# Kernel tuning notes

Hardware: AMD Instinct MI355X
Metric: run time of the kernel (lower is better)

Reference implementation:

```python
import jax, jax.numpy as jnp
import numpy as np

D_MODEL = 2048
N_HEADS = 16
D_K = D_MODEL // N_HEADS
MAX_SEQ_LEN = 2048


def _rotary_tables(dim, max_seq_len):
    angular_freq = (1.0 / 10000.0) ** jnp.linspace(0.0, 1.0, dim // 2, dtype=jnp.float32)
    t = jnp.arange(max_seq_len, dtype=jnp.float32)
    theta = jnp.einsum('i,j->ij', t, angular_freq)  # [S, dk/2]
    return jnp.cos(theta), jnp.sin(theta)


def _apply_rotary(x, cos, sin):
    # x: [B, H, S, dk]; cos/sin: [S, dk/2]
    seq_len = x.shape[-2]
    c = cos[:seq_len][None, None]
    s = sin[:seq_len][None, None]
    x1, x2 = jnp.split(x, 2, axis=-1)
    y1 = x1 * c - x2 * s
    y2 = x1 * s + x2 * c
    return jnp.concatenate([y1, y2], axis=-1).astype(x.dtype)


def setup_inputs() -> dict:
    key = jax.random.key(0)
    k_x, k_qkv, k_o = jax.random.split(key, 3)
    B, S = 2, 2048
    x = jax.random.normal(k_x, (B, S, D_MODEL), dtype=jnp.float32)
    scale = 1.0 / np.sqrt(D_MODEL)
    w_qkv = jax.random.normal(k_qkv, (3 * D_MODEL, D_MODEL), dtype=jnp.float32) * scale
    w_o = jax.random.normal(k_o, (D_MODEL, D_MODEL), dtype=jnp.float32) * scale
    return {"x": x, "w_qkv": w_qkv, "w_o": w_o}


def reference(x, w_qkv, w_o):
    B, S, _ = x.shape
    cos, sin = _rotary_tables(D_K, MAX_SEQ_LEN)
    qkv = jnp.einsum('bsd,ed->bse', x, w_qkv)  # [B, S, 3*d_model]
    qkv = qkv.reshape(B, S, 3, N_HEADS, D_K).transpose(2, 0, 3, 1, 4)  # [3,B,H,S,dk]
    Q, K, V = qkv[0], qkv[1], qkv[2]
    Q = _apply_rotary(Q, cos, sin)
    K = _apply_rotary(K, cos, sin)
    scale = 1.0 / np.sqrt(D_K)
    scores = jnp.einsum('bhqd,bhkd->bhqk', Q, K) * scale
    causal = jnp.tril(jnp.ones((S, S), dtype=bool))
    scores = jnp.where(causal[None, None], scores, jnp.finfo(scores.dtype).min)
    attn = jax.nn.softmax(scores, axis=-1)
    out = jnp.einsum('bhqk,bhkd->bhqd', attn, V)  # [B,H,S,dk]
    out = out.transpose(0, 2, 1, 3).reshape(B, S, D_MODEL)
    return jnp.einsum('bsd,ed->bse', out, w_o)
```

## Files before the change

kernel.cpp:

```cpp
#include <hip/hip_runtime.h>
#include <hip/hip_bf16.h>


typedef __bf16 bf16;
typedef __bf16 bf16x4 __attribute__((ext_vector_type(4)));
typedef __bf16 bf16x8 __attribute__((ext_vector_type(8)));
typedef float f32x4 __attribute__((ext_vector_type(4)));
typedef float f32x16 __attribute__((ext_vector_type(16)));
typedef int i32x4 __attribute__((ext_vector_type(4)));

#define DEV __device__ __forceinline__

DEV void gll16(const void* g, void* lds_base_wave_uniform) {
  __builtin_amdgcn_global_load_lds((const __attribute__((address_space(1))) void*)g,
                                   (__attribute__((address_space(3))) void*)lds_base_wave_uniform,
                                   16, 0, 0);
}

DEV f32x4 mfma16(bf16x8 a, bf16x8 b, f32x4 c) {
  return __builtin_amdgcn_mfma_f32_16x16x32_bf16(a, b, c, 0, 0, 0);
}
DEV f32x16 mfma32(bf16x8 a, bf16x8 b, f32x16 c) {
  return __builtin_amdgcn_mfma_f32_32x32x16_bf16(a, b, c, 0, 0, 0);
}

DEV int cvtpk(float lo, float hi) {
  int r;
  asm("v_cvt_pk_bf16_f32 %0, %1, %2" : "=v"(r) : "v"(lo), "v"(hi));
  return r;
}

__global__ __launch_bounds__(256) void prep_all(const float* __restrict__ x,
                                                const float* __restrict__ wqkv,
                                                const float* __restrict__ wo,
                                                bf16* __restrict__ xb,
                                                bf16* __restrict__ wqkvb,
                                                bf16* __restrict__ wob,
                                                float* __restrict__ ctab,
                                                float* __restrict__ stab) {
  const int b = blockIdx.x;
  if (b < 12288) {
    const float* in;
    bf16* out;
    int bb = b;
    if (b < 4096) {
      in = x; out = xb;
    } else if (b < 10240) {
      in = wqkv; out = wqkvb; bb -= 4096;
    } else {
      in = wo; out = wob; bb -= 10240;
    }
    const int i = (bb * 256 + threadIdx.x) << 3;
    float4 a = *(const float4*)(in + i);
    float4 c = *(const float4*)(in + i + 4);
    bf16x8 o;
    o[0] = (bf16)a.x; o[1] = (bf16)a.y; o[2] = (bf16)a.z; o[3] = (bf16)a.w;
    o[4] = (bf16)c.x; o[5] = (bf16)c.y; o[6] = (bf16)c.z; o[7] = (bf16)c.w;
    *(bf16x8*)(out + i) = o;
  } else {
    const int id = (b - 12288) * 256 + threadIdx.x;
    const int s = id >> 6, j = id & 63;
    float freq = powf(10000.0f, -(float)j / 63.0f);
    float th = (float)s * freq;
    ctab[id] = cosf(th);
    stab[id] = sinf(th);
  }
}

__global__ __launch_bounds__(512, 2) void gemm384(const bf16* __restrict__ A,
                                                  const bf16* __restrict__ Bt,
                                                  bf16* __restrict__ q_out,
                                                  bf16* __restrict__ k_out,
                                                  bf16* __restrict__ v_out,
                                                  const float* __restrict__ ctab,
                                                  const float* __restrict__ stab) {
  constexpr int K = 2048, NKT = 64;
  constexpr int BUFB = 40960;
  __shared__ char lds[3 * BUFB];
  const int id = blockIdx.x;
  const int swz = (id & 7) * 32 + (id >> 3);
  const int bx = swz & 15, by = swz >> 4;
  const int m0 = by << 8;
  const int n0 = bx * 384;
  const int tid = threadIdx.x, w = tid >> 6, l = tid & 63;
  const int wm = w >> 2, wn = w & 3;
  const int lsl = (l & 7) ^ ((l >> 3) & 7);
  const int srow = ((l >> 3) << 1) + (lsl >> 2);
  const int scol = (lsl & 3) << 3;

  auto STAGE = [&](int t, char* base) {
    const int k0 = t << 5;
#pragma unroll
    for (int c = 0; c < 2; ++c) {
      const int row = (c << 7) + (w << 4) + srow;
      gll16(A + (size_t)(m0 + row) * K + k0 + scol, base + (c << 13) + (w << 10));
    }
#pragma unroll
    for (int c = 0; c < 3; ++c) {
      const int row = (c << 7) + (w << 4) + srow;
      gll16(Bt + (size_t)(n0 + row) * K + k0 + scol, base + 16384 + (c << 13) + (w << 10));
    }
  };

  f32x4 acc[8][6] = {};

  STAGE(0, (char*)lds);
  STAGE(1, (char*)lds + BUFB);
  asm volatile("s_waitcnt vmcnt(5)" ::: "memory");
  __builtin_amdgcn_s_barrier();

#pragma unroll 1
  for (int t = 0, bi = 0, bj = 2; t < NKT; ++t) {
    char* rbase = (char*)lds + bi * BUFB;
    bf16x8 bfr[6];
#pragma unroll
    for (int j = 0; j < 6; ++j) {
      const int row = ((j >> 1) << 7) + ((j & 1) << 6) + (wn << 4) + (l & 15);
      const int sr = row >> 1;
      bfr[j] = *(const bf16x8*)(rbase + 16384 + sr * 128 +
                                (((((row & 1) << 2) | (l >> 4)) ^ (sr & 7)) << 4));
    }
    bf16x8 af[4];
#pragma unroll
    for (int i = 0; i < 4; ++i) {
      const int row = (wm << 7) + (i << 4) + (l & 15);
      const int sr = row >> 1;
      af[i] = *(const bf16x8*)(rbase + sr * 128 +
                               (((((row & 1) << 2) | (l >> 4)) ^ (sr & 7)) << 4));
    }
    if (t + 2 < NKT) STAGE(t + 2, (char*)lds + bj * BUFB);
    asm volatile("s_waitcnt lgkmcnt(0)" ::: "memory");
    __builtin_amdgcn_sched_barrier(0);
    __builtin_amdgcn_s_setprio(1);
#pragma unroll
    for (int i = 0; i < 4; ++i)
#pragma unroll
      for (int j = 0; j < 6; ++j)
        acc[i][j] = mfma16(af[i], bfr[j], acc[i][j]);
    __builtin_amdgcn_s_setprio(0);
#pragma unroll
    for (int i = 0; i < 4; ++i) {
      const int row = (wm << 7) + 64 + (i << 4) + (l & 15);
      const int sr = row >> 1;
      af[i] = *(const bf16x8*)(rbase + sr * 128 +
                               (((((row & 1) << 2) | (l >> 4)) ^ (sr & 7)) << 4));
    }
    asm volatile("s_waitcnt lgkmcnt(0)" ::: "memory");
    __builtin_amdgcn_sched_barrier(0);
    __builtin_amdgcn_s_setprio(1);
#pragma unroll
    for (int i = 0; i < 4; ++i)
#pragma unroll
      for (int j = 0; j < 6; ++j)
        acc[4 + i][j] = mfma16(af[i], bfr[j], acc[4 + i][j]);
    __builtin_amdgcn_s_setprio(0);
    if (t + 2 < NKT) {
      asm volatile("s_waitcnt vmcnt(5)" ::: "memory");
    } else if (t + 2 == NKT) {
      asm volatile("s_waitcnt vmcnt(0)" ::: "memory");
    }
    __builtin_amdgcn_sched_barrier(0);
    __builtin_amdgcn_s_barrier();
    bi = (bi == 2) ? 0 : bi + 1;
    bj = (bj == 2) ? 0 : bj + 1;
  }

  const int d2 = (wn << 4) + (l & 15);
#pragma unroll
  for (int i = 0; i < 8; ++i) {
    const int mbase = m0 + (wm << 7) + (i << 4) + ((l >> 4) << 2);
    const int b_ = mbase >> 11, sbase = mbase & 2047;
    float cc[4], ss[4];
    if (((n0 + 256) >> 11) == 1 || (n0 >> 11) == 1) {
#pragma unroll
      for (int r = 0; r < 4; ++r) {
        cc[r] = ctab[((sbase + r) << 6) + d2];
        ss[r] = stab[((sbase + r) << 6) + d2];
      }
    }
#pragma unroll
    for (int p = 0; p < 3; ++p) {
      const int nb = n0 + (p << 7);
      const int which = nb >> 11;
      const int h = (nb >> 7) & 15;
      if (which == 0) {
        const size_t base = (((size_t)((b_ << 4) | h)) * 2048 + sbase) * 128;
#pragma unroll
        for (int r = 0; r < 4; ++r) {
          q_out[base + ((size_t)r << 7) + d2]      = (bf16)acc[i][2 * p][r];
          q_out[base + ((size_t)r << 7) + d2 + 64] = (bf16)acc[i][2 * p + 1][r];
        }
      } else if (which == 1) {
        const size_t base = (((size_t)((b_ << 4) | h)) * 2048 + sbase) * 128;
#pragma unroll
        for (int r = 0; r < 4; ++r) {
          const float x1 = acc[i][2 * p][r], x2 = acc[i][2 * p + 1][r];
          k_out[base + ((size_t)r << 7) + d2]      = (bf16)(x1 * cc[r] - x2 * ss[r]);
          k_out[base + ((size_t)r << 7) + d2 + 64] = (bf16)(x1 * ss[r] + x2 * cc[r]);
        }
      } else {
        bf16x4 v1, v2;
#pragma unroll
        for (int r = 0; r < 4; ++r) {
          v1[r] = (bf16)acc[i][2 * p][r];
          v2[r] = (bf16)acc[i][2 * p + 1][r];
        }
        const size_t hb = ((size_t)((b_ << 4) | h) << 18);
        *(bf16x4*)(v_out + hb + ((size_t)d2 << 11) + sbase) = v1;
        *(bf16x4*)(v_out + hb + ((size_t)(d2 + 64) << 11) + sbase) = v2;
      }
    }
  }
}

template <int NTN>
__global__ __launch_bounds__(256, 2) void gemm_o(const bf16* __restrict__ A,
                                                 const bf16* __restrict__ Bt,
                                                 float* __restrict__ f_out) {
  constexpr int K = 2048, NKT = 64;
  constexpr int BUFB = 16384;
  __shared__ char lds[3 * BUFB];
  const int nwg = 32 * NTN;
  const int id = blockIdx.x;
  const int swz = (id & 7) * (nwg >> 3) + (id >> 3);
  const int bx = swz % NTN, by = swz / NTN;
  const int m0 = by << 7, n0 = bx << 7;
  const int tid = threadIdx.x, w = tid >> 6, l = tid & 63;
  const int wm = w >> 1, wn = w & 1;
  const int lsl = (l & 7) ^ ((l >> 3) & 7);
  const int srow = ((l >> 3) << 1) + (lsl >> 2);
  const int scol = (lsl & 3) << 3;

  auto STAGE = [&](int t, char* base) {
    const int k0 = t << 5;
#pragma unroll
    for (int c = 0; c < 2; ++c) {
      const int row = (c << 6) + (w << 4) + srow;
      gll16(A + (size_t)(m0 + row) * K + k0 + scol, base + (c << 12) + (w << 10));
      gll16(Bt + (size_t)(n0 + row) * K + k0 + scol, base + 8192 + (c << 12) + (w << 10));
    }
  };

  f32x4 acc[4][4] = {};

  STAGE(0, (char*)lds);
  STAGE(1, (char*)lds + BUFB);
  asm volatile("s_waitcnt vmcnt(4)" ::: "memory");
  __builtin_amdgcn_s_barrier();

#pragma unroll 1
  for (int t = 0, bi = 0, bj = 2; t < NKT; ++t) {
    char* rbase = (char*)lds + bi * BUFB;
    bf16x8 af[4], bfr[4];
#pragma unroll
    for (int i = 0; i < 4; ++i) {
      const int row = (wm << 6) + (i << 4) + (l & 15);
      const int sr = row >> 1;
      af[i] = *(const bf16x8*)(rbase + sr * 128 +
                               (((((row & 1) << 2) | (l >> 4)) ^ (sr & 7)) << 4));
    }
#pragma unroll
    for (int j = 0; j < 4; ++j) {
      const int row = (wn << 6) + (j << 4) + (l & 15);
      const int sr = row >> 1;
      bfr[j] = *(const bf16x8*)(rbase + 8192 + sr * 128 +
                                (((((row & 1) << 2) | (l >> 4)) ^ (sr & 7)) << 4));
    }
    if (t + 2 < NKT) STAGE(t + 2, (char*)lds + bj * BUFB);
    asm volatile("s_waitcnt lgkmcnt(0)" ::: "memory");
    __builtin_amdgcn_sched_barrier(0);
    __builtin_amdgcn_s_setprio(1);
#pragma unroll
    for (int i = 0; i < 4; ++i)
#pragma unroll
      for (int j = 0; j < 4; ++j)
        acc[i][j] = mfma16(af[i], bfr[j], acc[i][j]);
    __builtin_amdgcn_s_setprio(0);
    if (t + 2 < NKT) {
      asm volatile("s_waitcnt vmcnt(4)" ::: "memory");
    } else if (t + 2 == NKT) {
      asm volatile("s_waitcnt vmcnt(0)" ::: "memory");
    }
    __builtin_amdgcn_sched_barrier(0);
    __builtin_amdgcn_s_barrier();
    bi = (bi == 2) ? 0 : bi + 1;
    bj = (bj == 2) ? 0 : bj + 1;
  }

#pragma unroll
  for (int i = 0; i < 4; ++i)
#pragma unroll
    for (int j = 0; j < 4; ++j)
#pragma unroll
      for (int r = 0; r < 4; ++r) {
        const int m = m0 + (wm << 6) + (i << 4) + ((l >> 4) << 2) + r;
        const int n = n0 + (wn << 6) + (j << 4) + (l & 15);
        f_out[(size_t)m * 2048 + n] = acc[i][j][r];
      }
}

__global__ __launch_bounds__(512, 2) void attn_kernel(const bf16* __restrict__ Qb,
                                                      const bf16* __restrict__ Kb,
                                                      const bf16* __restrict__ Vt,
                                                      bf16* __restrict__ Ao,
                                                      const float* __restrict__ ctab,
                                                      const float* __restrict__ stab) {
  constexpr int S = 2048;
  __shared__ char lds[2][65536];
  const int id = blockIdx.x;
  const int swz = (id & 7) * 32 + (id >> 3);
  const int bh = swz >> 3;
  const int pp = swz & 7;
  const int ntA = pp + 1;
  const int NT = 17;
  const int tid = threadIdx.x, w = tid >> 6, l = tid & 63;
  const int wq = w & 3, half = w >> 2;
  const int hi = l >> 5;
  const bf16* Qp = Qb + ((size_t)bh << 18);
  const bf16* Kp = Kb + ((size_t)bh << 18);
  const bf16* Vp = Vt + ((size_t)bh << 18);

  auto KVSEQ = [&](int ti) { return ((ti < ntA) ? ti : ti - ntA) << 7; };

  auto STAGE_KV = [&](int kv0, int bufi) {
    char* Kbase = lds[bufi];
    char* Vbase = lds[bufi] + 32768;
#pragma unroll
    for (int i = 0; i < 2; ++i) {
      const int rk = (w << 4) + (i << 3) + ((l >> 4) << 1) + (i == 0 ? 0 : 0);
      (void)rk;
    }
#pragma unroll
    for (int i = 0; i < 2; ++i) {
    }
#pragma unroll
    for (int i = 0; i < 2; ++i) {
      const int r0 = (w << 4) + (i << 3) + (l >> 4);
      const int r1 = r0 + 4;
      gll16(Kp + ((size_t)(kv0 + r0) << 7) + (((l & 15) ^ (r0 & 7)) << 3),
            Kbase + (w << 12) + (i << 11));
      gll16(Kp + ((size_t)(kv0 + r1) << 7) + (((l & 15) ^ (r1 & 7)) << 3),
            Kbase + (w << 12) + (i << 11) + 1024);
      gll16(Vp + (size_t)r0 * S + kv0 + (((l & 15) ^ (r0 & 7)) << 3),
            Vbase + (w << 12) + (i << 11));
      gll16(Vp + (size_t)r1 * S + kv0 + (((l & 15) ^ (r1 & 7)) << 3),
            Vbase + (w << 12) + (i << 11) + 1024);
    }
  };

  bf16x8 qf[8];
  auto LOAD_Q = [&](int q0_) {
    const int sq = q0_ + (wq << 5) + (l & 31);
#pragma unroll
    for (int kt = 0; kt < 8; ++kt)
      qf[kt] = *(const bf16x8*)(Qp + ((size_t)sq << 7) + (kt << 4) + (hi << 3));
    const float QS = 0.08838834764831845f * 1.4426950408889634f;
#pragma unroll
    for (int kt = 0; kt < 4; ++kt) {
      const int d2 = (kt << 4) + (hi << 3);
      const float* cp = ctab + (sq << 6) + d2;
      const float* sp = stab + (sq << 6) + d2;
      float4 c0 = *(const float4*)cp, c1 = *(const float4*)(cp + 4);
      float4 s0 = *(const float4*)sp, s1 = *(const float4*)(sp + 4);
      const float cA[8] = {c0.x, c0.y, c0.z, c0.w, c1.x, c1.y, c1.z, c1.w};
      const float sA[8] = {s0.x, s0.y, s0.z, s0.w, s1.x, s1.y, s1.z, s1.w};
      const bf16x8 lo = qf[kt], up = qf[kt + 4];
#pragma unroll
      for (int j2 = 0; j2 < 8; ++j2) {
        const float a = (float)lo[j2], b2 = (float)up[j2];
        qf[kt][j2]     = (bf16)((a * cA[j2] - b2 * sA[j2]) * QS);
        qf[kt + 4][j2] = (bf16)((a * sA[j2] + b2 * cA[j2]) * QS);
      }
    }
  };

  f32x16 o[4] = {};
  float mrun = -3e38f, lrun = 0.f;
  int q0 = pp << 7;

  auto MERGE_EPI = [&](int q0_, char* scratch) {
    bf16* ob = (bf16*)scratch;
    float* ml = (float*)(scratch + 36864);
    __syncthreads();
    if (half == 1) {
      bf16* dst = ob + ((wq << 6) + l) * 72;
#pragma unroll
      for (int dt = 0; dt < 4; ++dt) {
        bf16x8 t0, t1;
#pragma unroll
        for (int e = 0; e < 8; ++e) { t0[e] = (bf16)o[dt][e]; t1[e] = (bf16)o[dt][8 + e]; }
        *(bf16x8*)(dst + (dt << 4)) = t0;
        *(bf16x8*)(dst + (dt << 4) + 8) = t1;
      }
      if (l < 32) {
        ml[(wq << 5) + l] = mrun;
        ml[128 + (wq << 5) + l] = lrun;
      }
    }
    __syncthreads();
    if (half == 0) {
      const float mhi = ml[(wq << 5) + (l & 31)];
      const float lhi = ml[128 + (wq << 5) + (l & 31)];
      const float ms = fmaxf(mrun, mhi);
      const float alo = exp2f(mrun - ms), ahi = exp2f(mhi - ms);
      const float rinv = 1.0f / (lrun * alo + lhi * ahi);
      const bf16* src = ob + ((wq << 6) + l) * 72;
      const int b = bh >> 4, h = bh & 15;
      const int sq = q0_ + (wq << 5) + (l & 31);
      bf16* Arow = Ao + (((size_t)(b * S + sq)) << 11) + (h << 7);
#pragma unroll
      for (int dt = 0; dt < 4; ++dt) {
        bf16x8 h0 = *(const bf16x8*)(src + (dt << 4));
        bf16x8 h1 = *(const bf16x8*)(src + (dt << 4) + 8);
#pragma unroll
        for (int g = 0; g < 4; ++g) {
          bf16x4 ov;
#pragma unroll
          for (int r = 0; r < 4; ++r) {
            const int e = (g << 2) + r;
            const float hv = (e < 8) ? (float)h0[e] : (float)h1[e - 8];
            ov[r] = (bf16)((o[dt][e] * alo + hv * ahi) * rinv);
          }
          *(bf16x4*)(Arow + (dt << 5) + (g << 3) + (hi << 2)) = ov;
        }
      }
    }
  };

  STAGE_KV(KVSEQ(0), 0);
  LOAD_Q(q0);
  __syncthreads();

  int bufi = 0;
#pragma unroll 1
  for (int ti = 0; ti < NT; ++ti, bufi ^= 1) {
    if (ti + 1 < NT) STAGE_KV(KVSEQ(ti + 1), bufi ^ 1);
    const int kv0 = KVSEQ(ti);
    const int kvh0 = kv0 + (half << 6);
    const int qminw = q0 + (wq << 5);
    if (kvh0 <= qminw + 31) {
      const char* Kbase = lds[bufi];
      const char* Vbase = lds[bufi] + 32768;
      f32x16 sc0 = {}, sc1 = {};
      __builtin_amdgcn_s_setprio(1);
#pragma unroll
      for (int kt = 0; kt < 8; ++kt) {
        const int rk0 = (l & 31) + (half << 6);
        const int coff = (kt << 5) + (hi << 4);
        bf16x8 k0 = *(const bf16x8*)(Kbase + (rk0 << 8) + (coff ^ ((rk0 & 7) << 4)));
        bf16x8 k1 = *(const bf16x8*)(Kbase + ((rk0 + 32) << 8) + (coff ^ (((rk0 + 32) & 7) << 4)));
        sc0 = mfma32(k0, qf[kt], sc0);
        sc1 = mfma32(k1, qf[kt], sc1);
      }
      __builtin_amdgcn_s_setprio(0);
      if (kvh0 + 63 > qminw) {
        const int qg = qminw + (l & 31);
#pragma unroll
        for (int r = 0; r < 16; ++r) {
          const int kvr = kvh0 + (r & 3) + ((r >> 2) << 3) + (hi << 2);
          if (kvr > qg) sc0[r] = -3e38f;
          if (kvr + 32 > qg) sc1[r] = -3e38f;
        }
      }
      f32x16 mm;
#pragma unroll
      for (int r = 0; r < 16; ++r) mm[r] = fmaxf(sc0[r], sc1[r]);
#pragma unroll
      for (int off = 8; off; off >>= 1)
#pragma unroll
        for (int r = 0; r < off; ++r) mm[r] = fmaxf(mm[r], mm[r + off]);
      float mx = mm[0];
      mx = fmaxf(mx, __shfl_xor(mx, 32));
      const float mnew = fmaxf(mrun, mx);
      if (!__all(mx <= mrun)) {
        const float alpha = exp2f(mrun - mnew);
        lrun *= alpha;
#pragma unroll
        for (int dt = 0; dt < 4; ++dt) o[dt] *= alpha;
      }
      mrun = mnew;
      float p0 = 0.f, p1 = 0.f, p2 = 0.f, p3 = 0.f;
#pragma unroll
      for (int r = 0; r < 16; r += 2) {
        sc0[r] = exp2f(sc0[r] - mnew); sc0[r + 1] = exp2f(sc0[r + 1] - mnew);
        sc1[r] = exp2f(sc1[r] - mnew); sc1[r + 1] = exp2f(sc1[r + 1] - mnew);
        p0 += sc0[r]; p1 += sc0[r + 1]; p2 += sc1[r]; p3 += sc1[r + 1];
      }
      float ps = (p0 + p1) + (p2 + p3);
      ps += __shfl_xor(ps, 32);
      lrun += ps;
#pragma unroll
      for (int ks = 0; ks < 4; ++ks) {
        const f32x16& s = (ks & 2) ? sc1 : sc0;
        const int rbp = (ks & 1) << 3;
        int pa_ = cvtpk(s[rbp + 0], s[rbp + 1]);
        int pb_ = cvtpk(s[rbp + 2], s[rbp + 3]);
        int pc_ = cvtpk(s[rbp + 4], s[rbp + 5]);
        int pd_ = cvtpk(s[rbp + 6], s[rbp + 7]);
        int sa = __shfl_xor(pa_, 32), sb2 = __shfl_xor(pb_, 32);
        int sc_ = __shfl_xor(pc_, 32), sd = __shfl_xor(pd_, 32);
        i32x4 pi;
        pi[0] = hi ? sc_ : pa_;
        pi[1] = hi ? sd : pb_;
        pi[2] = hi ? pc_ : sa;
        pi[3] = hi ? pd_ : sb2;
        const bf16x8 pf = __builtin_bit_cast(bf16x8, pi);
        __builtin_amdgcn_s_setprio(1);
#pragma unroll
        for (int dt = 0; dt < 4; ++dt) {
          const int rd = (dt << 5) + (l & 31);
          const int coffv = (half << 7) + (ks << 5) + (hi << 4);
          const bf16x8 vf = *(const bf16x8*)(Vbase + (rd << 8) +
                                             (coffv ^ ((rd & 7) << 4)));
          o[dt] = mfma32(vf, pf, o[dt]);
        }
        __builtin_amdgcn_s_setprio(0);
      }
    }
    if (ti == ntA - 1) {
      MERGE_EPI(q0, lds[bufi]);
      q0 = (15 - pp) << 7;
#pragma unroll
      for (int dt = 0; dt < 4; ++dt)
#pragma unroll
        for (int r = 0; r < 16; ++r) o[dt][r] = 0.f;
      mrun = -3e38f; lrun = 0.f;
      LOAD_Q(q0);
    }
    __syncthreads();
  }
  MERGE_EPI(q0, lds[(NT - 1) & 1]);
}

extern "C" void kernel_launch(void* const* d_in, const int* in_sizes, int n_in,
                              void* d_out, int out_size, void* d_ws, size_t ws_size,
                              hipStream_t stream) {
  const float* x = (const float*)d_in[0];
  const float* w_qkv = (const float*)d_in[1];
  const float* w_o = (const float*)d_in[2];
  float* out = (float*)d_out;
  char* ws = (char*)d_ws;

  bf16* xb    = (bf16*)(ws);
  bf16* wqkvb = (bf16*)(ws + (16ull << 20));
  bf16* wob   = (bf16*)(ws + (40ull << 20));
  bf16* Qb    = (bf16*)(ws + (48ull << 20));
  bf16* Kb    = (bf16*)(ws + (64ull << 20));
  bf16* Vt    = (bf16*)(ws + (80ull << 20));
  bf16* Ao    = (bf16*)(ws + (96ull << 20));
  float* ctab = (float*)(ws + (112ull << 20));
  float* stab = (float*)(ws + (113ull << 20));

  prep_all<<<12800, 256, 0, stream>>>(x, w_qkv, w_o, xb, wqkvb, wob, ctab, stab);
  gemm384<<<256, 512, 0, stream>>>(xb, wqkvb, Qb, Kb, Vt, ctab, stab);
  attn_kernel<<<256, 512, 0, stream>>>(Qb, Kb, Vt, Ao, ctab, stab);
  gemm_o<16><<<512, 256, 0, stream>>>(Ao, wob, out);
}
```

Baseline: 227.4 us.

## Halve attention KV tile to 64 rows to fit more blocks per CU

Shrinks each staged K/V tile from 128 to 64 keys, halving LDS per buffer so four 512-thread blocks can share a CU instead of two, and doubles the number of KV iterations. Each half-block now processes 32 keys with a single score accumulator, which cuts register pressure. The merge scratch is re-laid out with an XOR swizzle, and the max/sum values get their own small shared buffer. The cost is more loop iterations, more barriers and more staging overhead per tile, and the higher occupancy target may force register spills.

```diff
diff --git a/kernel.cpp b/kernel.cpp
--- a/kernel.cpp
+++ b/kernel.cpp
@@ -299,20 +299,21 @@
       }
 }
 
-__global__ __launch_bounds__(512, 2) void attn_kernel(const bf16* __restrict__ Qb,
+__global__ __launch_bounds__(512, 4) void attn_kernel(const bf16* __restrict__ Qb,
                                                       const bf16* __restrict__ Kb,
                                                       const bf16* __restrict__ Vt,
                                                       bf16* __restrict__ Ao,
                                                       const float* __restrict__ ctab,
                                                       const float* __restrict__ stab) {
   constexpr int S = 2048;
-  __shared__ char lds[2][65536];
+  __shared__ char lds[2][32768];
+  __shared__ float mlbuf[256];
   const int id = blockIdx.x;
   const int swz = (id & 7) * 32 + (id >> 3);
   const int bh = swz >> 3;
   const int pp = swz & 7;
-  const int ntA = pp + 1;
-  const int NT = 17;
+  const int ntA = (pp + 1) << 1;
+  const int NT = 34;
   const int tid = threadIdx.x, w = tid >> 6, l = tid & 63;
   const int wq = w & 3, half = w >> 2;
   const int hi = l >> 5;
@@ -320,31 +321,19 @@
   const bf16* Kp = Kb + ((size_t)bh << 18);
   const bf16* Vp = Vt + ((size_t)bh << 18);
 
-  auto KVSEQ = [&](int ti) { return ((ti < ntA) ? ti : ti - ntA) << 7; };
+  auto KVSEQ = [&](int ti) { return ((ti < ntA) ? ti : ti - ntA) << 6; };
 
   auto STAGE_KV = [&](int kv0, int bufi) {
     char* Kbase = lds[bufi];
-    char* Vbase = lds[bufi] + 32768;
+    char* Vbase = lds[bufi] + 16384;
 #pragma unroll
     for (int i = 0; i < 2; ++i) {
-      const int rk = (w << 4) + (i << 3) + ((l >> 4) << 1) + (i == 0 ? 0 : 0);
-      (void)rk;
-    }
-#pragma unroll
-    for (int i = 0; i < 2; ++i) {
-    }
-#pragma unroll
-    for (int i = 0; i < 2; ++i) {
-      const int r0 = (w << 4) + (i << 3) + (l >> 4);
-      const int r1 = r0 + 4;
-      gll16(Kp + ((size_t)(kv0 + r0) << 7) + (((l & 15) ^ (r0 & 7)) << 3),
-            Kbase + (w << 12) + (i << 11));
-      gll16(Kp + ((size_t)(kv0 + r1) << 7) + (((l & 15) ^ (r1 & 7)) << 3),
-            Kbase + (w << 12) + (i << 11) + 1024);
-      gll16(Vp + (size_t)r0 * S + kv0 + (((l & 15) ^ (r0 & 7)) << 3),
-            Vbase + (w << 12) + (i << 11));
-      gll16(Vp + (size_t)r1 * S + kv0 + (((l & 15) ^ (r1 & 7)) << 3),
-            Vbase + (w << 12) + (i << 11) + 1024);
+      const int rk = (w << 3) + (i << 2) + (l >> 4);
+      gll16(Kp + ((size_t)(kv0 + rk) << 7) + (((l & 15) ^ (rk & 7)) << 3),
+            Kbase + (w << 11) + (i << 10));
+      const int rv = (w << 4) + (i << 3) + (l >> 3);
+      gll16(Vp + (size_t)rv * S + kv0 + (((l & 7) ^ (rv & 7)) << 3),
+            Vbase + (w << 11) + (i << 10));
     }
   };
 
@@ -379,39 +368,37 @@
   int q0 = pp << 7;
 
   auto MERGE_EPI = [&](int q0_, char* scratch) {
-    bf16* ob = (bf16*)scratch;
-    float* ml = (float*)(scratch + 36864);
     __syncthreads();
     if (half == 1) {
-      bf16* dst = ob + ((wq << 6) + l) * 72;
+      char* dst = scratch + (((wq << 6) + l) << 7);
 #pragma unroll
       for (int dt = 0; dt < 4; ++dt) {
         bf16x8 t0, t1;
 #pragma unroll
         for (int e = 0; e < 8; ++e) { t0[e] = (bf16)o[dt][e]; t1[e] = (bf16)o[dt][8 + e]; }
-        *(bf16x8*)(dst + (dt << 4)) = t0;
-        *(bf16x8*)(dst + (dt << 4) + 8) = t1;
+        *(bf16x8*)(dst + ((((dt << 1) + 0) << 4) ^ ((l & 7) << 4))) = t0;
+        *(bf16x8*)(dst + ((((dt << 1) + 1) << 4) ^ ((l & 7) << 4))) = t1;
       }
       if (l < 32) {
-        ml[(wq << 5) + l] = mrun;
-        ml[128 + (wq << 5) + l] = lrun;
+        mlbuf[(wq << 5) + l] = mrun;
+        mlbuf[128 + (wq << 5) + l] = lrun;
       }
     }
     __syncthreads();
     if (half == 0) {
-      const float mhi = ml[(wq << 5) + (l & 31)];
-      const float lhi = ml[128 + (wq << 5) + (l & 31)];
+      const float mhi = mlbuf[(wq << 5) + (l & 31)];
+      const float lhi = mlbuf[128 + (wq << 5) + (l & 31)];
       const float ms = fmaxf(mrun, mhi);
       const float alo = exp2f(mrun - ms), ahi = exp2f(mhi - ms);
       const float rinv = 1.0f / (lrun * alo + lhi * ahi);
-      const bf16* src = ob + ((wq << 6) + l) * 72;
+      const char* src = scratch + (((wq << 6) + l) << 7);
       const int b = bh >> 4, h = bh & 15;
       const int sq = q0_ + (wq << 5) + (l & 31);
       bf16* Arow = Ao + (((size_t)(b * S + sq)) << 11) + (h << 7);
 #pragma unroll
       for (int dt = 0; dt < 4; ++dt) {
-        bf16x8 h0 = *(const bf16x8*)(src + (dt << 4));
-        bf16x8 h1 = *(const bf16x8*)(src + (dt << 4) + 8);
+        bf16x8 h0 = *(const bf16x8*)(src + ((((dt << 1) + 0) << 4) ^ ((l & 7) << 4)));
+        bf16x8 h1 = *(const bf16x8*)(src + ((((dt << 1) + 1) << 4) ^ ((l & 7) << 4)));
 #pragma unroll
         for (int g = 0; g < 4; ++g) {
           bf16x4 ov;
@@ -436,35 +423,30 @@
   for (int ti = 0; ti < NT; ++ti, bufi ^= 1) {
     if (ti + 1 < NT) STAGE_KV(KVSEQ(ti + 1), bufi ^ 1);
     const int kv0 = KVSEQ(ti);
-    const int kvh0 = kv0 + (half << 6);
+    const int kvh0 = kv0 + (half << 5);
     const int qminw = q0 + (wq << 5);
     if (kvh0 <= qminw + 31) {
       const char* Kbase = lds[bufi];
-      const char* Vbase = lds[bufi] + 32768;
-      f32x16 sc0 = {}, sc1 = {};
+      const char* Vbase = lds[bufi] + 16384;
+      f32x16 sc = {};
       __builtin_amdgcn_s_setprio(1);
 #pragma unroll
       for (int kt = 0; kt < 8; ++kt) {
-        const int rk0 = (l & 31) + (half << 6);
+        const int rk0 = (l & 31) + (half << 5);
         const int coff = (kt << 5) + (hi << 4);
-        bf16x8 k0 = *(const bf16x8*)(Kbase + (rk0 << 8) + (coff ^ ((rk0 & 7) << 4)));
-        bf16x8 k1 = *(const bf16x8*)(Kbase + ((rk0 + 32) << 8) + (coff ^ (((rk0 + 32) & 7) << 4)));
-        sc0 = mfma32(k0, qf[kt], sc0);
-        sc1 = mfma32(k1, qf[kt], sc1);
+        bf16x8 kf = *(const bf16x8*)(Kbase + (rk0 << 8) + (coff ^ ((rk0 & 7) << 4)));
+        sc = mfma32(kf, qf[kt], sc);
       }
       __builtin_amdgcn_s_setprio(0);
-      if (kvh0 + 63 > qminw) {
+      if (kvh0 + 31 > qminw) {
         const int qg = qminw + (l & 31);
 #pragma unroll
         for (int r = 0; r < 16; ++r) {
           const int kvr = kvh0 + (r & 3) + ((r >> 2) << 3) + (hi << 2);
-          if (kvr > qg) sc0[r] = -3e38f;
-          if (kvr + 32 > qg) sc1[r] = -3e38f;
+          if (kvr > qg) sc[r] = -3e38f;
         }
       }
-      f32x16 mm;
-#pragma unroll
-      for (int r = 0; r < 16; ++r) mm[r] = fmaxf(sc0[r], sc1[r]);
+      f32x16 mm = sc;
 #pragma unroll
       for (int off = 8; off; off >>= 1)
 #pragma unroll
@@ -479,24 +461,23 @@
         for (int dt = 0; dt < 4; ++dt) o[dt] *= alpha;
       }
       mrun = mnew;
-      float p0 = 0.f, p1 = 0.f, p2 = 0.f, p3 = 0.f;
+      float p0 = 0.f, p1 = 0.f;
 #pragma unroll
       for (int r = 0; r < 16; r += 2) {
-        sc0[r] = exp2f(sc0[r] - mnew); sc0[r + 1] = exp2f(sc0[r + 1] - mnew);
-        sc1[r] = exp2f(sc1[r] - mnew); sc1[r + 1] = exp2f(sc1[r + 1] - mnew);
-        p0 += sc0[r]; p1 += sc0[r + 1]; p2 += sc1[r]; p3 += sc1[r + 1];
-      }
-      float ps = (p0 + p1) + (p2 + p3);
+        sc[r] = exp2f(sc[r] - mnew);
+        sc[r + 1] = exp2f(sc[r + 1] - mnew);
+        p0 += sc[r]; p1 += sc[r + 1];
+      }
+      float ps = p0 + p1;
       ps += __shfl_xor(ps, 32);
       lrun += ps;
 #pragma unroll
-      for (int ks = 0; ks < 4; ++ks) {
-        const f32x16& s = (ks & 2) ? sc1 : sc0;
-        const int rbp = (ks & 1) << 3;
-        int pa_ = cvtpk(s[rbp + 0], s[rbp + 1]);
-        int pb_ = cvtpk(s[rbp + 2], s[rbp + 3]);
-        int pc_ = cvtpk(s[rbp + 4], s[rbp + 5]);
-        int pd_ = cvtpk(s[rbp + 6], s[rbp + 7]);
+      for (int ks = 0; ks < 2; ++ks) {
+        const int rbp = ks << 3;
+        int pa_ = cvtpk(sc[rbp + 0], sc[rbp + 1]);
+        int pb_ = cvtpk(sc[rbp + 2], sc[rbp + 3]);
+        int pc_ = cvtpk(sc[rbp + 4], sc[rbp + 5]);
+        int pd_ = cvtpk(sc[rbp + 6], sc[rbp + 7]);
         int sa = __shfl_xor(pa_, 32), sb2 = __shfl_xor(pb_, 32);
         int sc_ = __shfl_xor(pc_, 32), sd = __shfl_xor(pd_, 32);
         i32x4 pi;
@@ -509,8 +490,8 @@
 #pragma unroll
         for (int dt = 0; dt < 4; ++dt) {
           const int rd = (dt << 5) + (l & 31);
-          const int coffv = (half << 7) + (ks << 5) + (hi << 4);
-          const bf16x8 vf = *(const bf16x8*)(Vbase + (rd << 8) +
+          const int coffv = (half << 6) + (ks << 5) + (hi << 4);
+          const bf16x8 vf = *(const bf16x8*)(Vbase + (rd << 7) +
                                              (coffv ^ ((rd & 7) << 4)));
           o[dt] = mfma32(vf, pf, o[dt]);
         }
```

Measured after the change: 372.1 us. 1.64x slower.
